# Optimization experiments

Hardware: AMD Instinct MI355X
Metric: run time of the kernel (lower is better)

Reference implementation:

```python
import jax, jax.numpy as jnp
import numpy as np

WEIGHT_THRESH = 0.5
EPS = 1e-5
B, N = 4096, 1024


def setup_inputs() -> dict:
    key = jax.random.key(0)
    k1, k2, k3 = jax.random.split(key, 3)
    src = jax.random.normal(k1, (B, N, 3), dtype=jnp.float32)
    tgt = jax.random.normal(k2, (B, N, 3), dtype=jnp.float32)
    w = jax.random.uniform(k3, (B, N), dtype=jnp.float32)
    return {"src_points": src, "tgt_points": tgt, "weights": w}


def _weighted_procrustes(src, ref, w):
    # threshold + normalize weights
    w = jnp.where(w < WEIGHT_THRESH, jnp.zeros_like(w), w)
    w = w / (jnp.sum(w, axis=1, keepdims=True) + EPS)
    w = w[:, :, None]                       # (B, N, 1)
    # weighted centroids
    src_c = jnp.sum(src * w, axis=1, keepdims=True)   # (B, 1, 3)
    ref_c = jnp.sum(ref * w, axis=1, keepdims=True)   # (B, 1, 3)
    src0 = src - src_c
    ref0 = ref - ref_c
    # weighted cross-covariance H = src0^T @ (w * ref0): (B, 3, 3)
    H = jnp.einsum('bni,bnj->bij', src0, w * ref0)
    U, S, Vh = jnp.linalg.svd(H)            # torch.svd returns V, jnp returns Vh
    V = jnp.swapaxes(Vh, 1, 2)
    Ut = jnp.swapaxes(U, 1, 2)
    det = jnp.linalg.det(V @ Ut)            # (B,)
    sgn = jnp.sign(det)
    # D = diag(1, 1, sign(det)); V @ D scales the last column of V
    D = jnp.stack([jnp.ones_like(sgn), jnp.ones_like(sgn), sgn], axis=-1)  # (B, 3)
    R = (V * D[:, None, :]) @ Ut            # (B, 3, 3)
    # t = ref_c - R @ src_c
    t = (jnp.swapaxes(ref_c, 1, 2) - R @ jnp.swapaxes(src_c, 1, 2))[:, :, 0]  # (B, 3)
    return R, t


def reference(src_points, tgt_points, weights):
    return _weighted_procrustes(src_points, tgt_points, weights)
```

## Files before the change

### kernel.cpp

```cpp
#include <hip/hip_runtime.h>
#include <math.h>

#define WTHRESH 0.5f
#define EPSV    1e-5f

template <int CTRL>
__device__ __forceinline__ float dpp_add(float x) {
  int xi = __builtin_bit_cast(int, x);
  int mv = __builtin_amdgcn_update_dpp(0, xi, CTRL, 0xF, 0xF, true);
  return x + __builtin_bit_cast(float, mv);
}

#define JROT(app,aqq,apq, arp,arq, vAp,vAq, vBp,vBq, vCp,vCq)                 \
  do {                                                                        \
    float _apq = (apq);                                                       \
    if (fabsf(_apq) > 1e-30f) {                                               \
      float _tau = ((aqq) - (app)) * 0.5f / _apq;                             \
      float _t = copysignf(1.0f, _tau) / (fabsf(_tau) + sqrtf(1.0f + _tau*_tau)); \
      float _c = 1.0f / sqrtf(1.0f + _t*_t);                                  \
      float _s = _t * _c;                                                     \
      float _app = (app), _aqq = (aqq);                                       \
      (app) = _app - _t * _apq;                                               \
      (aqq) = _aqq + _t * _apq;                                               \
      (apq) = 0.0f;                                                           \
      float _arp = (arp), _arq = (arq);                                       \
      (arp) = _c * _arp - _s * _arq;                                          \
      (arq) = _s * _arp + _c * _arq;                                          \
      { float _vp=(vAp), _vq=(vAq); (vAp)=_c*_vp-_s*_vq; (vAq)=_s*_vp+_c*_vq; } \
      { float _vp=(vBp), _vq=(vBq); (vBp)=_c*_vp-_s*_vq; (vBq)=_s*_vp+_c*_vq; } \
      { float _vp=(vCp), _vq=(vCq); (vCp)=_c*_vp-_s*_vq; (vCq)=_s*_vp+_c*_vq; } \
    }                                                                         \
  } while (0)

#define CSWAP(li,lj, x0,x1, y0,y1, z0,z1)                                     \
  do { if ((li) < (lj)) {                                                     \
    float _t;                                                                 \
    _t=(li); (li)=(lj); (lj)=_t;                                              \
    _t=(x0); (x0)=(x1); (x1)=_t;                                              \
    _t=(y0); (y0)=(y1); (y1)=_t;                                              \
    _t=(z0); (z0)=(z1); (z1)=_t;                                              \
  } } while (0)

__global__ __launch_bounds__(256) void wproc_reduce(
    const float* __restrict__ src, const float* __restrict__ tgt,
    const float* __restrict__ wts, float* __restrict__ ws)
{
  const int b   = blockIdx.x;
  const int tid = threadIdx.x;

  const float4* s4 = reinterpret_cast<const float4*>(src + (size_t)b * 3072);
  const float4* t4 = reinterpret_cast<const float4*>(tgt + (size_t)b * 3072);
  const float4* w4 = reinterpret_cast<const float4*>(wts + (size_t)b * 1024);

  float4 sA = s4[3*tid+0], sB = s4[3*tid+1], sC = s4[3*tid+2];
  float4 tA = t4[3*tid+0], tB = t4[3*tid+1], tC = t4[3*tid+2];
  float4 wv = w4[tid];

  float acc[16];
  #pragma unroll
  for (int k = 0; k < 16; ++k) acc[k] = 0.0f;

  float PX[4][3] = {{sA.x,sA.y,sA.z},{sA.w,sB.x,sB.y},{sB.z,sB.w,sC.x},{sC.y,sC.z,sC.w}};
  float PY[4][3] = {{tA.x,tA.y,tA.z},{tA.w,tB.x,tB.y},{tB.z,tB.w,tC.x},{tC.y,tC.z,tC.w}};
  float WW[4]    = {wv.x, wv.y, wv.z, wv.w};

  #pragma unroll
  for (int k = 0; k < 4; ++k) {
    float w  = (WW[k] < WTHRESH) ? 0.0f : WW[k];
    float x0 = PX[k][0], x1 = PX[k][1], x2 = PX[k][2];
    float y0 = PY[k][0], y1 = PY[k][1], y2 = PY[k][2];
    acc[0] += w;
    acc[1] += w*x0; acc[2] += w*x1; acc[3] += w*x2;
    acc[4] += w*y0; acc[5] += w*y1; acc[6] += w*y2;
    float wx0 = w*x0, wx1 = w*x1, wx2 = w*x2;
    acc[7]  += wx0*y0; acc[8]  += wx0*y1; acc[9]  += wx0*y2;
    acc[10] += wx1*y0; acc[11] += wx1*y1; acc[12] += wx1*y2;
    acc[13] += wx2*y0; acc[14] += wx2*y1; acc[15] += wx2*y2;
  }

  #pragma unroll
  for (int k = 0; k < 16; ++k) acc[k] = dpp_add<0x111>(acc[k]);
  #pragma unroll
  for (int k = 0; k < 16; ++k) acc[k] = dpp_add<0x112>(acc[k]);
  #pragma unroll
  for (int k = 0; k < 16; ++k) acc[k] = dpp_add<0x114>(acc[k]);
  #pragma unroll
  for (int k = 0; k < 16; ++k) acc[k] = dpp_add<0x118>(acc[k]);
  #pragma unroll
  for (int k = 0; k < 16; ++k) acc[k] = dpp_add<0x142>(acc[k]);
  #pragma unroll
  for (int k = 0; k < 16; ++k) acc[k] = dpp_add<0x143>(acc[k]);

  if ((tid & 63) == 63) {
    float* o = ws + ((size_t)b * 4 + (tid >> 6)) * 16;
    #pragma unroll
    for (int k = 0; k < 16; ++k) o[k] = acc[k];
  }
}

__global__ __launch_bounds__(256) void wproc_svd(
    const float* __restrict__ ws, float* __restrict__ outR,
    float* __restrict__ outT, int B)
{
  const int b = blockIdx.x * 256 + threadIdx.x;
  if (b >= B) return;

  const float* p = ws + (size_t)b * 64;
  float f[16];
  #pragma unroll
  for (int k = 0; k < 16; ++k) f[k] = p[k] + p[16 + k] + p[32 + k] + p[48 + k];

  const float inv  = 1.0f / (f[0] + EPSV);
  const float cx0 = f[1]*inv, cx1 = f[2]*inv, cx2 = f[3]*inv;
  const float cy0 = f[4]*inv, cy1 = f[5]*inv, cy2 = f[6]*inv;
  const float ssum = f[0] * inv;
  const float g = 2.0f - ssum;

  float H00 = f[7]*inv  - g*cx0*cy0, H01 = f[8]*inv  - g*cx0*cy1, H02 = f[9]*inv  - g*cx0*cy2;
  float H10 = f[10]*inv - g*cx1*cy0, H11 = f[11]*inv - g*cx1*cy1, H12 = f[12]*inv - g*cx1*cy2;
  float H20 = f[13]*inv - g*cx2*cy0, H21 = f[14]*inv - g*cx2*cy1, H22 = f[15]*inv - g*cx2*cy2;

  float a00 = H00*H00 + H10*H10 + H20*H20;
  float a11 = H01*H01 + H11*H11 + H21*H21;
  float a22 = H02*H02 + H12*H12 + H22*H22;
  float a01 = H00*H01 + H10*H11 + H20*H21;
  float a02 = H00*H02 + H10*H12 + H20*H22;
  float a12 = H01*H02 + H11*H12 + H21*H22;

  float v00=1.f,v01=0.f,v02=0.f, v10=0.f,v11=1.f,v12=0.f, v20=0.f,v21=0.f,v22=1.f;

  #pragma unroll
  for (int sweep = 0; sweep < 8; ++sweep) {
    JROT(a00,a11,a01, a02,a12, v00,v01, v10,v11, v20,v21);
    JROT(a00,a22,a02, a01,a12, v00,v02, v10,v12, v20,v22);
    JROT(a11,a22,a12, a01,a02, v01,v02, v11,v12, v21,v22);
  }

  CSWAP(a00,a11, v00,v01, v10,v11, v20,v21);
  CSWAP(a00,a22, v00,v02, v10,v12, v20,v22);
  CSWAP(a11,a22, v01,v02, v11,v12, v21,v22);

  float u00 = H00*v00 + H01*v10 + H02*v20;
  float u10 = H10*v00 + H11*v10 + H12*v20;
  float u20 = H20*v00 + H21*v10 + H22*v20;
  float u01 = H00*v01 + H01*v11 + H02*v21;
  float u11 = H10*v01 + H11*v11 + H12*v21;
  float u21 = H20*v01 + H21*v11 + H22*v21;
  float u02 = H00*v02 + H01*v12 + H02*v22;
  float u12 = H10*v02 + H11*v12 + H12*v22;
  float u22 = H20*v02 + H21*v12 + H22*v22;

  float n0 = sqrtf(u00*u00 + u10*u10 + u20*u20);
  float n1 = sqrtf(u01*u01 + u11*u11 + u21*u21);
  float n2 = sqrtf(u02*u02 + u12*u12 + u22*u22);

  float R00,R01,R02,R10,R11,R12,R20,R21,R22;

  if (n0 < 1e-20f) {
    R00=1.f;R01=0.f;R02=0.f; R10=0.f;R11=1.f;R12=0.f; R20=0.f;R21=0.f;R22=1.f;
  } else {
    float i0 = 1.0f / n0;
    u00*=i0; u10*=i0; u20*=i0;

    if (n1 > 1e-7f * n0) {
      float i1 = 1.0f / n1;
      u01*=i1; u11*=i1; u21*=i1;
    } else {
      float ax = fabsf(u00), ay = fabsf(u10), az = fabsf(u20);
      float e0,e1,e2;
      if (ax <= ay && ax <= az)      { e0=1.f; e1=0.f; e2=0.f; }
      else if (ay <= az)             { e0=0.f; e1=1.f; e2=0.f; }
      else                           { e0=0.f; e1=0.f; e2=1.f; }
      u01 = u10*e2 - u20*e1;
      u11 = u20*e0 - u00*e2;
      u21 = u00*e1 - u10*e0;
      float nn = 1.0f / sqrtf(u01*u01 + u11*u11 + u21*u21);
      u01*=nn; u11*=nn; u21*=nn;
    }

    if (n2 > 1e-7f * n0) {
      float i2 = 1.0f / n2;
      u02*=i2; u12*=i2; u22*=i2;
    } else {
      u02 = u10*u21 - u20*u11;
      u12 = u20*u01 - u00*u21;
      u22 = u00*u11 - u10*u01;
    }

    float detU = u00*(u11*u22 - u12*u21) - u01*(u10*u22 - u12*u20) + u02*(u10*u21 - u11*u20);
    float detV = v00*(v11*v22 - v12*v21) - v01*(v10*v22 - v12*v20) + v02*(v10*v21 - v11*v20);
    float sgn = (detU * detV < 0.0f) ? -1.0f : 1.0f;

    R00 = v00*u00 + v01*u01 + sgn*v02*u02;
    R01 = v00*u10 + v01*u11 + sgn*v02*u12;
    R02 = v00*u20 + v01*u21 + sgn*v02*u22;
    R10 = v10*u00 + v11*u01 + sgn*v12*u02;
    R11 = v10*u10 + v11*u11 + sgn*v12*u12;
    R12 = v10*u20 + v11*u21 + sgn*v12*u22;
    R20 = v20*u00 + v21*u01 + sgn*v22*u02;
    R21 = v20*u10 + v21*u11 + sgn*v22*u12;
    R22 = v20*u20 + v21*u21 + sgn*v22*u22;
  }

  float t0 = cy0 - (R00*cx0 + R01*cx1 + R02*cx2);
  float t1 = cy1 - (R10*cx0 + R11*cx1 + R12*cx2);
  float t2 = cy2 - (R20*cx0 + R21*cx1 + R22*cx2);

  float* Rb = outR + (size_t)b * 9;
  Rb[0]=R00; Rb[1]=R01; Rb[2]=R02;
  Rb[3]=R10; Rb[4]=R11; Rb[5]=R12;
  Rb[6]=R20; Rb[7]=R21; Rb[8]=R22;
  float* tb = outT + (size_t)b * 3;
  tb[0]=t0; tb[1]=t1; tb[2]=t2;
}

extern "C" void kernel_launch(void* const* d_in, const int* in_sizes, int n_in,
                              void* d_out, int out_size, void* d_ws, size_t ws_size,
                              hipStream_t stream) {
  const float* src = (const float*)d_in[0];
  const float* tgt = (const float*)d_in[1];
  const float* w   = (const float*)d_in[2];

  const int B = in_sizes[2] / 1024;
  float* outR = (float*)d_out;
  float* outT = outR + (size_t)B * 9;
  float* ws   = (float*)d_ws;

  wproc_reduce<<<dim3(B), dim3(256), 0, stream>>>(src, tgt, w, ws);
  wproc_svd<<<dim3((B + 255) / 256), dim3(256), 0, stream>>>(ws, outR, outT, B);
}
```

Baseline: 140.7 us.

## Map one wave per batch item with 16 points per lane in reduce

```diff
diff --git a/kernel.cpp b/kernel.cpp
--- a/kernel.cpp
+++ b/kernel.cpp
@@ -41,41 +41,52 @@
     _t=(z0); (z0)=(z1); (z1)=_t;                                              \
   } } while (0)
 
-__global__ __launch_bounds__(256) void wproc_reduce(
+__global__ __launch_bounds__(256, 2) void wproc_reduce(
     const float* __restrict__ src, const float* __restrict__ tgt,
     const float* __restrict__ wts, float* __restrict__ ws)
 {
-  const int b   = blockIdx.x;
-  const int tid = threadIdx.x;
-
-  const float4* s4 = reinterpret_cast<const float4*>(src + (size_t)b * 3072);
-  const float4* t4 = reinterpret_cast<const float4*>(tgt + (size_t)b * 3072);
-  const float4* w4 = reinterpret_cast<const float4*>(wts + (size_t)b * 1024);
-
-  float4 sA = s4[3*tid+0], sB = s4[3*tid+1], sC = s4[3*tid+2];
-  float4 tA = t4[3*tid+0], tB = t4[3*tid+1], tC = t4[3*tid+2];
-  float4 wv = w4[tid];
+  const int wave = threadIdx.x >> 6;
+  const int lane = threadIdx.x & 63;
+  const int b    = blockIdx.x * 4 + wave;
+
+  const float4* sg = reinterpret_cast<const float4*>(src + (size_t)b * 3072) + lane * 12;
+  const float4* tg = reinterpret_cast<const float4*>(tgt + (size_t)b * 3072) + lane * 12;
+  const float4* wg = reinterpret_cast<const float4*>(wts + (size_t)b * 1024) + lane * 4;
+
+  float4 S[12], T[12], W[4];
+  #pragma unroll
+  for (int i = 0; i < 12; ++i) S[i] = sg[i];
+  #pragma unroll
+  for (int i = 0; i < 12; ++i) T[i] = tg[i];
+  #pragma unroll
+  for (int i = 0; i < 4; ++i)  W[i] = wg[i];
 
   float acc[16];
   #pragma unroll
   for (int k = 0; k < 16; ++k) acc[k] = 0.0f;
 
-  float PX[4][3] = {{sA.x,sA.y,sA.z},{sA.w,sB.x,sB.y},{sB.z,sB.w,sC.x},{sC.y,sC.z,sC.w}};
-  float PY[4][3] = {{tA.x,tA.y,tA.z},{tA.w,tB.x,tB.y},{tB.z,tB.w,tC.x},{tC.y,tC.z,tC.w}};
-  float WW[4]    = {wv.x, wv.y, wv.z, wv.w};
-
-  #pragma unroll
-  for (int k = 0; k < 4; ++k) {
-    float w  = (WW[k] < WTHRESH) ? 0.0f : WW[k];
-    float x0 = PX[k][0], x1 = PX[k][1], x2 = PX[k][2];
-    float y0 = PY[k][0], y1 = PY[k][1], y2 = PY[k][2];
-    acc[0] += w;
-    acc[1] += w*x0; acc[2] += w*x1; acc[3] += w*x2;
-    acc[4] += w*y0; acc[5] += w*y1; acc[6] += w*y2;
-    float wx0 = w*x0, wx1 = w*x1, wx2 = w*x2;
-    acc[7]  += wx0*y0; acc[8]  += wx0*y1; acc[9]  += wx0*y2;
-    acc[10] += wx1*y0; acc[11] += wx1*y1; acc[12] += wx1*y2;
-    acc[13] += wx2*y0; acc[14] += wx2*y1; acc[15] += wx2*y2;
+  #pragma unroll
+  for (int g = 0; g < 4; ++g) {
+    float4 sA = S[3*g+0], sB = S[3*g+1], sC = S[3*g+2];
+    float4 tA = T[3*g+0], tB = T[3*g+1], tC = T[3*g+2];
+    float4 wv = W[g];
+    float PX[4][3] = {{sA.x,sA.y,sA.z},{sA.w,sB.x,sB.y},{sB.z,sB.w,sC.x},{sC.y,sC.z,sC.w}};
+    float PY[4][3] = {{tA.x,tA.y,tA.z},{tA.w,tB.x,tB.y},{tB.z,tB.w,tC.x},{tC.y,tC.z,tC.w}};
+    float WW[4]    = {wv.x, wv.y, wv.z, wv.w};
+
+    #pragma unroll
+    for (int k = 0; k < 4; ++k) {
+      float w  = (WW[k] < WTHRESH) ? 0.0f : WW[k];
+      float x0 = PX[k][0], x1 = PX[k][1], x2 = PX[k][2];
+      float y0 = PY[k][0], y1 = PY[k][1], y2 = PY[k][2];
+      acc[0] += w;
+      acc[1] += w*x0; acc[2] += w*x1; acc[3] += w*x2;
+      acc[4] += w*y0; acc[5] += w*y1; acc[6] += w*y2;
+      float wx0 = w*x0, wx1 = w*x1, wx2 = w*x2;
+      acc[7]  += wx0*y0; acc[8]  += wx0*y1; acc[9]  += wx0*y2;
+      acc[10] += wx1*y0; acc[11] += wx1*y1; acc[12] += wx1*y2;
+      acc[13] += wx2*y0; acc[14] += wx2*y1; acc[15] += wx2*y2;
+    }
   }
 
   #pragma unroll
@@ -91,10 +102,12 @@
   #pragma unroll
   for (int k = 0; k < 16; ++k) acc[k] = dpp_add<0x143>(acc[k]);
 
-  if ((tid & 63) == 63) {
-    float* o = ws + ((size_t)b * 4 + (tid >> 6)) * 16;
-    #pragma unroll
-    for (int k = 0; k < 16; ++k) o[k] = acc[k];
+  if (lane == 63) {
+    float4* o = reinterpret_cast<float4*>(ws + (size_t)b * 16);
+    o[0] = make_float4(acc[0],  acc[1],  acc[2],  acc[3]);
+    o[1] = make_float4(acc[4],  acc[5],  acc[6],  acc[7]);
+    o[2] = make_float4(acc[8],  acc[9],  acc[10], acc[11]);
+    o[3] = make_float4(acc[12], acc[13], acc[14], acc[15]);
   }
 }
 
@@ -105,10 +118,10 @@
   const int b = blockIdx.x * 256 + threadIdx.x;
   if (b >= B) return;
 
-  const float* p = ws + (size_t)b * 64;
-  float f[16];
-  #pragma unroll
-  for (int k = 0; k < 16; ++k) f[k] = p[k] + p[16 + k] + p[32 + k] + p[48 + k];
+  const float4* p4 = reinterpret_cast<const float4*>(ws + (size_t)b * 16);
+  float4 F0 = p4[0], F1 = p4[1], F2 = p4[2], F3 = p4[3];
+  float f[16] = {F0.x,F0.y,F0.z,F0.w, F1.x,F1.y,F1.z,F1.w,
+                 F2.x,F2.y,F2.z,F2.w, F3.x,F3.y,F3.z,F3.w};
 
   const float inv  = 1.0f / (f[0] + EPSV);
   const float cx0 = f[1]*inv, cx1 = f[2]*inv, cx2 = f[3]*inv;
@@ -226,6 +239,6 @@
   float* outT = outR + (size_t)B * 9;
   float* ws   = (float*)d_ws;
 
-  wproc_reduce<<<dim3(B), dim3(256), 0, stream>>>(src, tgt, w, ws);
+  wproc_reduce<<<dim3(B / 4), dim3(256), 0, stream>>>(src, tgt, w, ws);
   wproc_svd<<<dim3((B + 255) / 256), dim3(256), 0, stream>>>(ws, outR, outT, B);
 }
```

New measurement: 178.7 us. 27.0% more time.
